# Kernel optimization log

Hardware: AMD Instinct MI355X
Metric: run time of the kernel (lower is better)

## Reference

```python
import jax, jax.numpy as jnp
import numpy as np

S_SCALE = 40.0  # ReuseThreshold default s
EPS = 0.0  # torch .norm division has no eps; keep faithful


def _monotonic_threshold(param):
    # get_monotonic_threshold with use_sigmoid=True: squash raw param into (0, 1)
    return jax.nn.sigmoid(param)


def setup_inputs() -> dict:
    key = jax.random.key(0)
    k1, k2, k3, k4, k5 = jax.random.split(key, 5)
    B, N, D = 16, 2048, 768
    return {
        "query_input": jax.random.normal(k1, (B, N, D), dtype=jnp.float32),
        "query_value": jax.random.normal(k2, (B, N, D), dtype=jnp.float32),
        "cached_input": jax.random.normal(k3, (B, N, D), dtype=jnp.float32),
        "cached_value": jax.random.normal(k4, (B, N, D), dtype=jnp.float32),
        "sim_threshold": jax.random.normal(k5, (N,), dtype=jnp.float32),
    }


def reference(query_input, query_value, cached_input, cached_value, sim_threshold):
    # L2-normalize along feature dim
    nq = query_input / jnp.linalg.norm(query_input, axis=-1, keepdims=True)
    nc = cached_input / jnp.linalg.norm(cached_input, axis=-1, keepdims=True)
    # full similarity matrix [B, N, N], top-1 retrieval
    sim = jnp.einsum("bnd,bmd->bnm", nq, nc)
    most_similar_score = jnp.max(sim, axis=-1)          # [B, N]
    most_similar_idx = jnp.argmax(sim, axis=-1)         # [B, N]
    idx = most_similar_idx[..., None]                   # [B, N, 1]
    similar_input = jnp.take_along_axis(cached_input, idx, axis=1)  # [B, N, D]
    similar_value = jnp.take_along_axis(cached_value, idx, axis=1)
    # learned sigmoid threshold blend
    threshold = _monotonic_threshold(sim_threshold)     # [N]
    reuse_map = jax.nn.sigmoid(S_SCALE * (most_similar_score - threshold))  # [B, N]
    rm = reuse_map[..., None]
    reuse_input = (1.0 - rm) * query_input + rm * similar_input
    reuse_value = (1.0 - rm) * query_value + rm * similar_value
    return (reuse_map, reuse_input, reuse_value)
```

## Files before the change

kernel.cpp:

```cpp
#include <hip/hip_runtime.h>
#include <stdint.h>

#define BB 16
#define NN 2048
#define DD 768
#define BN (BB*NN)
#define NCH (DD/32)


typedef __attribute__((ext_vector_type(8))) short bf16x8;
typedef __attribute__((ext_vector_type(4))) float f32x4;

__device__ __forceinline__ ushort f2bf_rne(float x) {
    uint32_t u = __float_as_uint(x);
    u += 0x7fffu + ((u >> 16) & 1u);
    return (ushort)(u >> 16);
}

__device__ __forceinline__ void gload16(const void* g, void* l) {
    __builtin_amdgcn_global_load_lds(
        (const __attribute__((address_space(1))) void*)g,
        (__attribute__((address_space(3))) void*)l,
        16, 0, 0);
}

__global__ __launch_bounds__(256) void normconv_kernel(
        const float* __restrict__ qi, const float* __restrict__ ci,
        ushort* __restrict__ qh, ushort* __restrict__ ql,
        ushort* __restrict__ ch, ushort* __restrict__ cl) {
    int row  = blockIdx.x * 4 + (threadIdx.x >> 6);
    int lane = threadIdx.x & 63;
    bool isq = row < BN;
    const float* src = isq ? qi : ci;
    int r = row & (BN - 1);
    const float4* p = (const float4*)(src + (size_t)r * DD);
    float4 v[3];
    float s = 0.0f;
#pragma unroll
    for (int k = 0; k < 3; k++) {
        v[k] = p[lane + 64 * k];
        s += v[k].x*v[k].x + v[k].y*v[k].y + v[k].z*v[k].z + v[k].w*v[k].w;
    }
#pragma unroll
    for (int off = 32; off; off >>= 1) s += __shfl_xor(s, off);
    float inv = 1.0f / sqrtf(s);
    ushort* dh = (isq ? qh : ch) + (size_t)r * DD;
    ushort* dl = (isq ? ql : cl) + (size_t)r * DD;
#pragma unroll
    for (int k = 0; k < 3; k++) {
        int f = lane + 64 * k;
        float n[4] = {v[k].x * inv, v[k].y * inv, v[k].z * inv, v[k].w * inv};
        ushort hs[4], ls[4];
#pragma unroll
        for (int e = 0; e < 4; e++) {
            hs[e] = f2bf_rne(n[e]);
            ls[e] = f2bf_rne(n[e] - __uint_as_float((uint32_t)hs[e] << 16));
        }
        uint2 hv, lv;
        hv.x = (uint32_t)hs[0] | ((uint32_t)hs[1] << 16);
        hv.y = (uint32_t)hs[2] | ((uint32_t)hs[3] << 16);
        lv.x = (uint32_t)ls[0] | ((uint32_t)ls[1] << 16);
        lv.y = (uint32_t)ls[2] | ((uint32_t)ls[3] << 16);
        *(uint2*)(dh + 4 * (size_t)f) = hv;
        *(uint2*)(dl + 4 * (size_t)f) = lv;
    }
}

__global__ __launch_bounds__(256, 2) void simmax_kernel(
        const ushort* __restrict__ qh, const ushort* __restrict__ ql,
        const ushort* __restrict__ ch, const ushort* __restrict__ cl,
        float* __restrict__ pmax, int* __restrict__ pidx) {
    __shared__ ushort smem[2][4][128 * 32];
    __shared__ float  redm[2][128];
    __shared__ int    redi[2][128];

    const int t  = threadIdx.x;
    const int l  = t & 63, wid = t >> 6;
    const int wy = wid >> 1, wx = wid & 1;
    const int fr = l & 15,  fs = l >> 4;
    const int n0 = blockIdx.x * 128;
    const int ms = blockIdx.y;
    const int b  = blockIdx.z;
    const int n0g = b * NN + n0;

    const int rowl = l >> 2;
    const int gs   = (l & 3) ^ ((l >> 3) & 3);
    const int rb   = wid * 32;

    const int swz = (fs ^ ((fr >> 1) & 3)) * 8;
    const int ra0 = (wy * 64 + fr) * 32 + swz;
    const int rb0 = (wx * 64 + fr) * 32 + swz;

    const ushort* srcs[4] = {qh, ql, ch, cl};

    float rmax[16]; int ridx[16];
#pragma unroll
    for (int k = 0; k < 16; k++) { rmax[k] = -3.0e38f; ridx[k] = 0; }

    for (int mt = ms; mt < 16; mt += 4) {
        const int m0  = mt * 128;
        const int m0g = b * NN + m0;

        f32x4 acc[4][4];
#pragma unroll
        for (int i = 0; i < 4; i++)
#pragma unroll
            for (int j = 0; j < 4; j++)
#pragma unroll
                for (int r = 0; r < 4; r++) acc[i][j][r] = 0.0f;

#pragma unroll
        for (int a = 0; a < 4; a++) {
            const ushort* sp = srcs[a]
                + (size_t)((a < 2 ? n0g : m0g) + rb + rowl) * DD + gs * 8;
            ushort* lp = &smem[0][a][rb * 32];
            gload16(sp, lp);
            gload16(sp + 16 * DD, lp + 16 * 32);
        }
        __syncthreads();

        int cur = 0;
        for (int c = 0; c < NCH; c++) {
            if (c + 1 < NCH) {
                const int k1 = (c + 1) * 32;
#pragma unroll
                for (int a = 0; a < 4; a++) {
                    const ushort* sp = srcs[a]
                        + (size_t)((a < 2 ? n0g : m0g) + rb + rowl) * DD
                        + k1 + gs * 8;
                    ushort* lp = &smem[cur ^ 1][a][rb * 32];
                    gload16(sp, lp);
                    gload16(sp + 16 * DD, lp + 16 * 32);
                }
            }
            bf16x8 ah[4], al[4], bhf[4], blf[4];
#pragma unroll
            for (int i = 0; i < 4; i++) {
                ah[i]  = *(const bf16x8*)&smem[cur][0][ra0 + i * 512];
                al[i]  = *(const bf16x8*)&smem[cur][1][ra0 + i * 512];
                bhf[i] = *(const bf16x8*)&smem[cur][2][rb0 + i * 512];
                blf[i] = *(const bf16x8*)&smem[cur][3][rb0 + i * 512];
            }
#pragma unroll
            for (int i = 0; i < 4; i++)
#pragma unroll
                for (int j = 0; j < 4; j++) {
                    asm("v_mfma_f32_16x16x32_bf16 %0, %1, %2, %0"
                        : "+v"(acc[i][j]) : "v"(ah[i]), "v"(bhf[j]));
                    asm("v_mfma_f32_16x16x32_bf16 %0, %1, %2, %0"
                        : "+v"(acc[i][j]) : "v"(al[i]), "v"(bhf[j]));
                    asm("v_mfma_f32_16x16x32_bf16 %0, %1, %2, %0"
                        : "+v"(acc[i][j]) : "v"(ah[i]), "v"(blf[j]));
                }
            __syncthreads();
            cur ^= 1;
        }

#pragma unroll
        for (int j = 0; j < 4; j++) {
            const int col = m0 + wx * 64 + j * 16 + fr;
#pragma unroll
            for (int i = 0; i < 4; i++)
#pragma unroll
                for (int r = 0; r < 4; r++) {
                    float val = acc[i][j][r];
                    int k = i * 4 + r;
                    if (val > rmax[k]) { rmax[k] = val; ridx[k] = col; }
                }
        }
    }

#pragma unroll
    for (int k = 0; k < 16; k++) {
        float m = rmax[k]; int id2 = ridx[k];
#pragma unroll
        for (int off = 1; off < 16; off <<= 1) {
            float om = __shfl_xor(m, off);
            int   oi = __shfl_xor(id2, off);
            if (om > m || (om == m && oi < id2)) { m = om; id2 = oi; }
        }
        if (fr == 0) {
            int r_loc = wy * 64 + (k >> 2) * 16 + fs * 4 + (k & 3);
            redm[wx][r_loc] = m;
            redi[wx][r_loc] = id2;
        }
    }
    __syncthreads();
    if (t < 128) {
        float m0v = redm[0][t]; int i0 = redi[0][t];
        float m1v = redm[1][t]; int i1 = redi[1][t];
        if (m1v > m0v || (m1v == m0v && i1 < i0)) { m0v = m1v; i0 = i1; }
        pmax[(b * 4 + ms) * NN + n0 + t] = m0v;
        pidx[(b * 4 + ms) * NN + n0 + t] = i0;
    }
}

__global__ __launch_bounds__(256) void merge_kernel(
        const float* __restrict__ pmax, const int* __restrict__ pidx,
        const float* __restrict__ st,
        float* __restrict__ out_map,
        float* __restrict__ ws_rm, int* __restrict__ ws_idx) {
    int id = blockIdx.x * 256 + threadIdx.x;
    int b = id >> 11, n = id & 2047;
    float best = pmax[(b * 4) * NN + n];
    int   bi   = pidx[(b * 4) * NN + n];
#pragma unroll
    for (int s = 1; s < 4; s++) {
        float p = pmax[(b * 4 + s) * NN + n];
        int   q = pidx[(b * 4 + s) * NN + n];
        if (p > best || (p == best && q < bi)) { best = p; bi = q; }
    }
    float thr = 1.0f / (1.0f + expf(-st[n]));
    float rm  = 1.0f / (1.0f + expf(-40.0f * (best - thr)));
    out_map[id] = rm;
    ws_rm[id]   = rm;
    ws_idx[id]  = bi;
}

__global__ __launch_bounds__(256) void blend_kernel(
        const float* __restrict__ qi, const float* __restrict__ qv,
        const float* __restrict__ ci, const float* __restrict__ cv,
        const float* __restrict__ ws_rm, const int* __restrict__ ws_idx,
        float* __restrict__ out_ri, float* __restrict__ out_rv) {
    int row  = blockIdx.x * 4 + (threadIdx.x >> 6);
    int lane = threadIdx.x & 63;
    float rm  = ws_rm[row];
    int gidx  = ws_idx[row];
    int b     = row >> 11;
    float om  = 1.0f - rm;
    const float4* q4 = (const float4*)(qi + (size_t)row * DD);
    const float4* v4 = (const float4*)(qv + (size_t)row * DD);
    const float4* s4 = (const float4*)(ci + ((size_t)b * NN + gidx) * DD);
    const float4* w4 = (const float4*)(cv + ((size_t)b * NN + gidx) * DD);
    float4* ori = (float4*)(out_ri + (size_t)row * DD);
    float4* orv = (float4*)(out_rv + (size_t)row * DD);
#pragma unroll
    for (int k = 0; k < 3; k++) {
        int f = lane + 64 * k;
        float4 a = q4[f], si = s4[f];
        float4 o;
        o.x = om * a.x + rm * si.x;
        o.y = om * a.y + rm * si.y;
        o.z = om * a.z + rm * si.z;
        o.w = om * a.w + rm * si.w;
        ori[f] = o;
        float4 av = v4[f], sv = w4[f];
        float4 p;
        p.x = om * av.x + rm * sv.x;
        p.y = om * av.y + rm * sv.y;
        p.z = om * av.z + rm * sv.z;
        p.w = om * av.w + rm * sv.w;
        orv[f] = p;
    }
}

extern "C" void kernel_launch(void* const* d_in, const int* in_sizes, int n_in,
                              void* d_out, int out_size, void* d_ws, size_t ws_size,
                              hipStream_t stream) {
    const float* qi = (const float*)d_in[0];
    const float* qv = (const float*)d_in[1];
    const float* ci = (const float*)d_in[2];
    const float* cv = (const float*)d_in[3];
    const float* st = (const float*)d_in[4];

    float* ws    = (float*)d_ws;
    float* pmax  = ws;
    int*   pidx  = (int*)(ws + 131072);
    float* ws_rm = ws + 262144;
    int*   ws_id = (int*)(ws + 294912);

    float* out     = (float*)d_out;
    float* out_map = out;
    float* out_ri  = out + 32768;
    float* out_rv  = out + 32768 + (size_t)BN * DD;

    ushort* qh = (ushort*)out_ri;
    ushort* ql = qh + (size_t)BN * DD;
    ushort* ch = (ushort*)out_rv;
    ushort* cl = ch + (size_t)BN * DD;

    normconv_kernel<<<(2 * BN) / 4, 256, 0, stream>>>(qi, ci, qh, ql, ch, cl);
    dim3 g2(16, 4, BB);
    simmax_kernel<<<g2, 256, 0, stream>>>(qh, ql, ch, cl, pmax, pidx);
    merge_kernel<<<BN / 256, 256, 0, stream>>>(pmax, pidx, st,
                                               out_map, ws_rm, ws_id);
    blend_kernel<<<BN / 4, 256, 0, stream>>>(qi, qv, ci, cv, ws_rm, ws_id,
                                             out_ri, out_rv);
}
```

Before: 798.1 us.

## Load query operands directly from global in simmax and fuse merge into blend

The simmax kernel no longer stages the query hi/lo bf16 tiles through LDS. Each lane now reads its A fragments straight from global memory (L2/L1 cached), which halves the shared-memory footprint and lets launch bounds ask for 3 blocks per CU. The separate merge kernel is folded into the blend kernel, so each row's wave reduces the partial max/argmax itself, and one launch plus the workspace round-trip go away. The risk is that uncoalesced direct global fragment loads in the inner K loop add latency, which occupancy and the double-buffered B tile may not hide.

New measurement: 1.251 ms. 56.7% more time.

```diff
diff --git a/kernel.cpp b/kernel.cpp
--- a/kernel.cpp
+++ b/kernel.cpp
@@ -66,11 +66,11 @@
     }
 }
 
-__global__ __launch_bounds__(256, 2) void simmax_kernel(
+__global__ __launch_bounds__(256, 3) void simmax_kernel(
         const ushort* __restrict__ qh, const ushort* __restrict__ ql,
         const ushort* __restrict__ ch, const ushort* __restrict__ cl,
         float* __restrict__ pmax, int* __restrict__ pidx) {
-    __shared__ ushort smem[2][4][128 * 32];
+    __shared__ ushort smem[2][2][128 * 32];
     __shared__ float  redm[2][128];
     __shared__ int    redi[2][128];
 
@@ -88,10 +88,10 @@
     const int rb   = wid * 32;
 
     const int swz = (fs ^ ((fr >> 1) & 3)) * 8;
-    const int ra0 = (wy * 64 + fr) * 32 + swz;
     const int rb0 = (wx * 64 + fr) * 32 + swz;
 
-    const ushort* srcs[4] = {qh, ql, ch, cl};
+    const ushort* aH = qh + (size_t)(n0g + wy * 64 + fr) * DD + fs * 8;
+    const ushort* aL = ql + (size_t)(n0g + wy * 64 + fr) * DD + fs * 8;
 
     float rmax[16]; int ridx[16];
 #pragma unroll
@@ -109,13 +109,13 @@
 #pragma unroll
                 for (int r = 0; r < 4; r++) acc[i][j][r] = 0.0f;
 
-#pragma unroll
-        for (int a = 0; a < 4; a++) {
-            const ushort* sp = srcs[a]
-                + (size_t)((a < 2 ? n0g : m0g) + rb + rowl) * DD + gs * 8;
-            ushort* lp = &smem[0][a][rb * 32];
-            gload16(sp, lp);
-            gload16(sp + 16 * DD, lp + 16 * 32);
+        {
+            const ushort* spH = ch + (size_t)(m0g + rb + rowl) * DD + gs * 8;
+            const ushort* spL = cl + (size_t)(m0g + rb + rowl) * DD + gs * 8;
+            gload16(spH, &smem[0][0][rb * 32]);
+            gload16(spH + 16 * DD, &smem[0][0][rb * 32 + 16 * 32]);
+            gload16(spL, &smem[0][1][rb * 32]);
+            gload16(spL + 16 * DD, &smem[0][1][rb * 32 + 16 * 32]);
         }
         __syncthreads();
 
@@ -123,23 +123,24 @@
         for (int c = 0; c < NCH; c++) {
             if (c + 1 < NCH) {
                 const int k1 = (c + 1) * 32;
-#pragma unroll
-                for (int a = 0; a < 4; a++) {
-                    const ushort* sp = srcs[a]
-                        + (size_t)((a < 2 ? n0g : m0g) + rb + rowl) * DD
-                        + k1 + gs * 8;
-                    ushort* lp = &smem[cur ^ 1][a][rb * 32];
-                    gload16(sp, lp);
-                    gload16(sp + 16 * DD, lp + 16 * 32);
-                }
+                const ushort* spH = ch + (size_t)(m0g + rb + rowl) * DD + k1 + gs * 8;
+                const ushort* spL = cl + (size_t)(m0g + rb + rowl) * DD + k1 + gs * 8;
+                gload16(spH, &smem[cur ^ 1][0][rb * 32]);
+                gload16(spH + 16 * DD, &smem[cur ^ 1][0][rb * 32 + 16 * 32]);
+                gload16(spL, &smem[cur ^ 1][1][rb * 32]);
+                gload16(spL + 16 * DD, &smem[cur ^ 1][1][rb * 32 + 16 * 32]);
             }
+            const size_t kof = (size_t)c * 32;
             bf16x8 ah[4], al[4], bhf[4], blf[4];
 #pragma unroll
             for (int i = 0; i < 4; i++) {
-                ah[i]  = *(const bf16x8*)&smem[cur][0][ra0 + i * 512];
-                al[i]  = *(const bf16x8*)&smem[cur][1][ra0 + i * 512];
-                bhf[i] = *(const bf16x8*)&smem[cur][2][rb0 + i * 512];
-                blf[i] = *(const bf16x8*)&smem[cur][3][rb0 + i * 512];
+                ah[i] = *(const bf16x8*)(aH + (size_t)i * 16 * DD + kof);
+                al[i] = *(const bf16x8*)(aL + (size_t)i * 16 * DD + kof);
+            }
+#pragma unroll
+            for (int j = 0; j < 4; j++) {
+                bhf[j] = *(const bf16x8*)&smem[cur][0][rb0 + j * 512];
+                blf[j] = *(const bf16x8*)&smem[cur][1][rb0 + j * 512];
             }
 #pragma unroll
             for (int i = 0; i < 4; i++)
@@ -195,13 +196,17 @@
     }
 }
 
-__global__ __launch_bounds__(256) void merge_kernel(
+__global__ __launch_bounds__(256) void blend_kernel(
+        const float* __restrict__ qi, const float* __restrict__ qv,
+        const float* __restrict__ ci, const float* __restrict__ cv,
         const float* __restrict__ pmax, const int* __restrict__ pidx,
         const float* __restrict__ st,
         float* __restrict__ out_map,
-        float* __restrict__ ws_rm, int* __restrict__ ws_idx) {
-    int id = blockIdx.x * 256 + threadIdx.x;
-    int b = id >> 11, n = id & 2047;
+        float* __restrict__ out_ri, float* __restrict__ out_rv) {
+    int row  = blockIdx.x * 4 + (threadIdx.x >> 6);
+    int lane = threadIdx.x & 63;
+    int b = row >> 11, n = row & 2047;
+
     float best = pmax[(b * 4) * NN + n];
     int   bi   = pidx[(b * 4) * NN + n];
 #pragma unroll
@@ -212,21 +217,9 @@
     }
     float thr = 1.0f / (1.0f + expf(-st[n]));
     float rm  = 1.0f / (1.0f + expf(-40.0f * (best - thr)));
-    out_map[id] = rm;
-    ws_rm[id]   = rm;
-    ws_idx[id]  = bi;
-}
-
-__global__ __launch_bounds__(256) void blend_kernel(
-        const float* __restrict__ qi, const float* __restrict__ qv,
-        const float* __restrict__ ci, const float* __restrict__ cv,
-        const float* __restrict__ ws_rm, const int* __restrict__ ws_idx,
-        float* __restrict__ out_ri, float* __restrict__ out_rv) {
-    int row  = blockIdx.x * 4 + (threadIdx.x >> 6);
-    int lane = threadIdx.x & 63;
-    float rm  = ws_rm[row];
-    int gidx  = ws_idx[row];
-    int b     = row >> 11;
+    if (lane == 0) out_map[row] = rm;
+
+    int gidx  = bi;
     float om  = 1.0f - rm;
     const float4* q4 = (const float4*)(qi + (size_t)row * DD);
     const float4* v4 = (const float4*)(qv + (size_t)row * DD);
@@ -266,8 +259,6 @@
     float* ws    = (float*)d_ws;
     float* pmax  = ws;
     int*   pidx  = (int*)(ws + 131072);
-    float* ws_rm = ws + 262144;
-    int*   ws_id = (int*)(ws + 294912);
 
     float* out     = (float*)d_out;
     float* out_map = out;
@@ -282,8 +273,6 @@
     normconv_kernel<<<(2 * BN) / 4, 256, 0, stream>>>(qi, ci, qh, ql, ch, cl);
     dim3 g2(16, 4, BB);
     simmax_kernel<<<g2, 256, 0, stream>>>(qh, ql, ch, cl, pmax, pidx);
-    merge_kernel<<<BN / 256, 256, 0, stream>>>(pmax, pidx, st,
-                                               out_map, ws_rm, ws_id);
-    blend_kernel<<<BN / 4, 256, 0, stream>>>(qi, qv, ci, cv, ws_rm, ws_id,
-                                             out_ri, out_rv);
-}
+    blend_kernel<<<BN / 4, 256, 0, stream>>>(qi, qv, ci, cv, pmax, pidx, st,
+                                             out_map, out_ri, out_rv);
+}
```
